# Kernel tuning notes

Measured on AMD Instinct MI355X. Metric: run time of the kernel, lower is better.

Reference implementation:

```python
import jax, jax.numpy as jnp
import numpy as np

V_NUM = 100000
E_NUM = 50000
N_PAIRS = 600000
DIM = 128
TAU = 0.5

def setup_inputs() -> dict:
    key = jax.random.key(0)
    ks = jax.random.split(key, 8)
    v_fea = jax.random.normal(ks[0], (V_NUM, DIM), dtype=jnp.float32)
    t_fea = jax.random.normal(ks[1], (V_NUM, DIM), dtype=jnp.float32)
    e_fea = jax.random.normal(ks[2], (E_NUM, DIM), dtype=jnp.float32)
    # xavier-normal-ish init (gain sqrt(2), fan_in=DIM, fan_out=1)
    std = (2.0 ** 0.5) * (2.0 / (DIM + 1)) ** 0.5
    a_v = jax.random.normal(ks[3], (DIM, 1), dtype=jnp.float32) * std
    a_t = jax.random.normal(ks[4], (DIM, 1), dtype=jnp.float32) * std
    a_e = jax.random.normal(ks[5], (DIM, 1), dtype=jnp.float32) * std
    v_idx = jax.random.randint(ks[6], (N_PAIRS,), 0, V_NUM, dtype=jnp.int32)
    e_idx = jax.random.randint(ks[7], (N_PAIRS,), 0, E_NUM, dtype=jnp.int32)
    ve = jnp.stack([v_idx, e_idx], axis=1)  # [N_PAIRS, 2]
    return {"v_fea": v_fea, "t_fea": t_fea, "e_fea": e_fea,
            "a_v": a_v, "a_t": a_t, "a_e": a_e, "ve": ve}

def reference(v_fea, t_fea, e_fea, a_v, a_t, a_e, ve):
    v = ve[:, 0]
    e = ve[:, 1]
    # per-node / per-edge attention scalars  [*, 1]
    s_v = v_fea @ a_v
    s_t = t_fea @ a_t
    s_e = e_fea @ a_e
    # per-pair score: gather by v and e, tanh, temperature
    a = jnp.tanh(s_v[v] + s_t[v] + s_e[e]) / TAU  # [N_PAIRS, 1]
    # segment softmax over pairs grouped by vertex v
    a_max = jax.ops.segment_max(a, v, num_segments=V_NUM)  # [V_NUM, 1]
    ex = jnp.exp(a - jax.lax.stop_gradient(a_max)[v])
    denom = jax.ops.segment_sum(ex, v, num_segments=V_NUM)  # [V_NUM, 1]
    w = ex / denom[v]  # [N_PAIRS, 1]
    # weighted scatter-sum of edge features into vertices
    out = jax.ops.segment_sum(w * e_fea[e], v, num_segments=V_NUM)  # [V_NUM, DIM]
    return out
```

## Files before the change

kernel.cpp:

```cpp
#include <hip/hip_runtime.h>

#define V_NUM 100000
#define E_NUM 50000
#define N_PAIRS 600000
#define DIM 128
#define SCAN_BLK 1024
#define N_SCAN_BLOCKS ((V_NUM + SCAN_BLK - 1) / SCAN_BLK)

__global__ void scores_kernel(const float* __restrict__ v_fea,
                              const float* __restrict__ t_fea,
                              const float* __restrict__ e_fea,
                              const float* __restrict__ a_v,
                              const float* __restrict__ a_t,
                              const float* __restrict__ a_e,
                              float* __restrict__ s_vt,
                              float* __restrict__ s_e) {
    const int wave = (int)((blockIdx.x * blockDim.x + threadIdx.x) >> 6);
    const int lane = (int)(threadIdx.x & 63);
    if (wave >= V_NUM + E_NUM) return;

    float partial;
    if (wave < V_NUM) {
        const float2 vv = ((const float2*)(v_fea + (size_t)wave * DIM))[lane];
        const float2 tt = ((const float2*)(t_fea + (size_t)wave * DIM))[lane];
        const float2 wv = ((const float2*)a_v)[lane];
        const float2 wt = ((const float2*)a_t)[lane];
        partial = vv.x * wv.x + vv.y * wv.y + tt.x * wt.x + tt.y * wt.y;
    } else {
        const int r = wave - V_NUM;
        const float2 ee = ((const float2*)(e_fea + (size_t)r * DIM))[lane];
        const float2 we = ((const float2*)a_e)[lane];
        partial = ee.x * we.x + ee.y * we.y;
    }
    #pragma unroll
    for (int off = 32; off > 0; off >>= 1)
        partial += __shfl_xor(partial, off, 64);
    if (lane == 0) {
        if (wave < V_NUM) s_vt[wave] = partial;
        else s_e[wave - V_NUM] = partial;
    }
}

__global__ void pair_hist(const int* __restrict__ ve, int* __restrict__ counts) {
    const int p = (int)(blockIdx.x * blockDim.x + threadIdx.x);
    if (p >= N_PAIRS) return;
    const int v = ((const int2*)ve)[p].x;
    atomicAdd(&counts[v], 1);
}

__global__ void scan_blocks(const int* __restrict__ counts,
                            int* __restrict__ blk_scan,
                            int* __restrict__ aux) {
    __shared__ int sdata[256];
    const int tid = (int)threadIdx.x;
    const int base = (int)blockIdx.x * SCAN_BLK + tid * 4;
    int4 c = make_int4(0, 0, 0, 0);
    if (base + 3 < V_NUM) {
        c = *(const int4*)(counts + base);
    } else {
        if (base + 0 < V_NUM) c.x = counts[base + 0];
        if (base + 1 < V_NUM) c.y = counts[base + 1];
        if (base + 2 < V_NUM) c.z = counts[base + 2];
        if (base + 3 < V_NUM) c.w = counts[base + 3];
    }
    const int s = c.x + c.y + c.z + c.w;
    sdata[tid] = s;
    __syncthreads();
    #pragma unroll
    for (int off = 1; off < 256; off <<= 1) {
        const int val = (tid >= off) ? sdata[tid - off] : 0;
        __syncthreads();
        sdata[tid] += val;
        __syncthreads();
    }
    const int excl = sdata[tid] - s;
    if (tid == 255) aux[blockIdx.x] = sdata[255];
    const int e0 = excl;
    const int e1 = e0 + c.x;
    const int e2 = e1 + c.y;
    const int e3 = e2 + c.z;
    if (base + 3 < V_NUM) {
        *(int4*)(blk_scan + base) = make_int4(e0, e1, e2, e3);
    } else {
        if (base + 0 < V_NUM) blk_scan[base + 0] = e0;
        if (base + 1 < V_NUM) blk_scan[base + 1] = e1;
        if (base + 2 < V_NUM) blk_scan[base + 2] = e2;
    }
}

__global__ void scan_aux(int* __restrict__ aux ) {
    __shared__ int sdata[128];
    const int tid = (int)threadIdx.x;
    const int orig = (tid < N_SCAN_BLOCKS) ? aux[tid] : 0;
    sdata[tid] = orig;
    __syncthreads();
    #pragma unroll
    for (int off = 1; off < 128; off <<= 1) {
        const int val = (tid >= off) ? sdata[tid - off] : 0;
        __syncthreads();
        sdata[tid] += val;
        __syncthreads();
    }
    if (tid < N_SCAN_BLOCKS) aux[tid] = sdata[tid] - orig;
}

__global__ void pair_scatter(const int* __restrict__ ve,
                             const float* __restrict__ s_vt,
                             const float* __restrict__ s_e,
                             const int* __restrict__ blk_scan,
                             const int* __restrict__ aux_scan,
                             int* __restrict__ cursor,
                             int* __restrict__ csr_e,
                             float* __restrict__ csr_ex) {
    const int p = (int)(blockIdx.x * blockDim.x + threadIdx.x);
    if (p >= N_PAIRS) return;
    const int2 pe = ((const int2*)ve)[p];
    const int v = pe.x, e = pe.y;
    const float a = tanhf(s_vt[v] + s_e[e]) * 2.0f;
    const float ex = __expf(a);
    const int start = blk_scan[v] + aux_scan[v >> 10];
    const int pos = start + atomicAdd(&cursor[v], 1);
    csr_e[pos] = e;
    csr_ex[pos] = ex;
}

__global__ void csr_aggregate(const int* __restrict__ counts,
                              const int* __restrict__ blk_scan,
                              const int* __restrict__ aux_scan,
                              const int* __restrict__ csr_e,
                              const float* __restrict__ csr_ex,
                              const float* __restrict__ e_fea,
                              float* __restrict__ out) {
    const int v = (int)((blockIdx.x * blockDim.x + threadIdx.x) >> 6);
    const int lane = (int)(threadIdx.x & 63);
    if (v >= V_NUM) return;
    const int start = blk_scan[v] + aux_scan[v >> 10];
    const int cnt = counts[v];

    float denom = 0.0f;
    for (int i = 0; i < cnt; ++i) denom += csr_ex[start + i];
    const float inv = (cnt > 0) ? (1.0f / denom) : 0.0f;

    float2 acc = make_float2(0.0f, 0.0f);
    for (int i = 0; i < cnt; ++i) {
        const int e = csr_e[start + i];
        const float w = csr_ex[start + i] * inv;
        const float2 ef = ((const float2*)(e_fea + (size_t)e * DIM))[lane];
        acc.x += w * ef.x;
        acc.y += w * ef.y;
    }
    ((float2*)(out + (size_t)v * DIM))[lane] = acc;
}

extern "C" void kernel_launch(void* const* d_in, const int* in_sizes, int n_in,
                              void* d_out, int out_size, void* d_ws, size_t ws_size,
                              hipStream_t stream) {
    const float* v_fea = (const float*)d_in[0];
    const float* t_fea = (const float*)d_in[1];
    const float* e_fea = (const float*)d_in[2];
    const float* a_v   = (const float*)d_in[3];
    const float* a_t   = (const float*)d_in[4];
    const float* a_e   = (const float*)d_in[5];
    const int*   ve    = (const int*)d_in[6];
    float* out = (float*)d_out;

    char* ws = (char*)d_ws;
    float* s_vt     = (float*)(ws + 0);
    float* s_e      = (float*)(ws + 524288);
    int*   counts   = (int*)  (ws + 1048576);
    int*   cursor   = (int*)  (ws + 1048576 + 400000);
    int*   blk_scan = (int*)  (ws + 2097152);
    int*   aux_scan = (int*)  (ws + 2097152 + 400000);
    int*   csr_e    = (int*)  (ws + 3145728);
    float* csr_ex   = (float*)(ws + 6291456);

    hipMemsetAsync(counts, 0, 800000, stream);

    {
        const int total_waves = V_NUM + E_NUM;
        const int threads = 256;
        const int blocks = (total_waves * 64 + threads - 1) / threads;
        scores_kernel<<<blocks, threads, 0, stream>>>(v_fea, t_fea, e_fea,
                                                      a_v, a_t, a_e, s_vt, s_e);
    }
    pair_hist<<<(N_PAIRS + 255) / 256, 256, 0, stream>>>(ve, counts);
    scan_blocks<<<N_SCAN_BLOCKS, 256, 0, stream>>>(counts, blk_scan, aux_scan);
    scan_aux<<<1, 128, 0, stream>>>(aux_scan);
    pair_scatter<<<(N_PAIRS + 255) / 256, 256, 0, stream>>>(
        ve, s_vt, s_e, blk_scan, aux_scan, cursor, csr_e, csr_ex);
    {
        const int threads = 256;
        const long long total = (long long)V_NUM * 64;
        const int blocks = (int)((total + threads - 1) / threads);
        csr_aggregate<<<blocks, threads, 0, stream>>>(
            counts, blk_scan, aux_scan, csr_e, csr_ex, e_fea, out);
    }
}
```

Before: 331.9 us.

## Fuse pipeline into one cooperative persistent kernel with grid syncs

Replaces the memset and six separate launches with a single cooperative kernel. It zeroes counts, computes scores, builds the histogram, scans, scatters into the CSR and aggregates, with grid.sync between phases, and keeps the multi-kernel path as a fallback. The CSR entries are packed as int2 (edge, ex) pairs. The aggregation now loads 64 entries per wave at once and broadcasts them with shuffles, which replaces the serial per-lane scalar loads and the separate denominator pass. The aim is to remove launch overhead and the duplicate CSR reads. The cost is a grid-stride persistent schedule and cooperative-launch grid barriers.

After: 1.026 ms. 3.09x slower.

```diff
diff --git a/kernel.cpp b/kernel.cpp
--- a/kernel.cpp
+++ b/kernel.cpp
@@ -1,4 +1,7 @@
 #include <hip/hip_runtime.h>
+#include <hip/hip_cooperative_groups.h>
+
+namespace cg = cooperative_groups;
 
 #define V_NUM 100000
 #define E_NUM 50000
@@ -6,19 +9,152 @@
 #define DIM 128
 #define SCAN_BLK 1024
 #define N_SCAN_BLOCKS ((V_NUM + SCAN_BLK - 1) / SCAN_BLK)
-
-__global__ void scores_kernel(const float* __restrict__ v_fea,
-                              const float* __restrict__ t_fea,
-                              const float* __restrict__ e_fea,
-                              const float* __restrict__ a_v,
-                              const float* __restrict__ a_t,
-                              const float* __restrict__ a_e,
-                              float* __restrict__ s_vt,
-                              float* __restrict__ s_e) {
+#define NTHREADS 256
+
+__global__ __launch_bounds__(NTHREADS, 4)
+void fused_kernel(const float* __restrict__ v_fea, const float* __restrict__ t_fea,
+                  const float* __restrict__ e_fea, const float* __restrict__ a_v,
+                  const float* __restrict__ a_t, const float* __restrict__ a_e,
+                  const int* __restrict__ ve, float* __restrict__ out,
+                  float* __restrict__ s_vt, float* __restrict__ s_e,
+                  int* __restrict__ counts, int* __restrict__ cursor,
+                  int* __restrict__ blk_scan, int* __restrict__ aux_scan,
+                  int2* __restrict__ csr) {
+    cg::grid_group grid = cg::this_grid();
+    __shared__ int sdata[NTHREADS];
+
+    const int tid = (int)(blockIdx.x * blockDim.x + threadIdx.x);
+    const int nthreads = (int)(gridDim.x * blockDim.x);
+    const int lane = (int)(threadIdx.x & 63);
+    const int wid = tid >> 6;
+    const int nwaves = nthreads >> 6;
+
+    {
+        int4* z = (int4*)counts;
+        for (int i = tid; i < 50000; i += nthreads) z[i] = make_int4(0, 0, 0, 0);
+    }
+    {
+        const float2 wv = ((const float2*)a_v)[lane];
+        const float2 wt = ((const float2*)a_t)[lane];
+        const float2 we = ((const float2*)a_e)[lane];
+        for (int row = wid; row < V_NUM + E_NUM; row += nwaves) {
+            float partial;
+            if (row < V_NUM) {
+                const float2 vv = ((const float2*)(v_fea + (size_t)row * DIM))[lane];
+                const float2 tt = ((const float2*)(t_fea + (size_t)row * DIM))[lane];
+                partial = vv.x * wv.x + vv.y * wv.y + tt.x * wt.x + tt.y * wt.y;
+            } else {
+                const int r = row - V_NUM;
+                const float2 ee = ((const float2*)(e_fea + (size_t)r * DIM))[lane];
+                partial = ee.x * we.x + ee.y * we.y;
+            }
+            #pragma unroll
+            for (int off = 32; off; off >>= 1) partial += __shfl_xor(partial, off, 64);
+            if (lane == 0) {
+                if (row < V_NUM) s_vt[row] = partial;
+                else s_e[row - V_NUM] = partial;
+            }
+        }
+    }
+    grid.sync();
+
+    for (int p = tid; p < N_PAIRS; p += nthreads)
+        atomicAdd(&counts[((const int2*)ve)[p].x], 1);
+    grid.sync();
+
+    if (blockIdx.x < N_SCAN_BLOCKS) {
+        const int t = (int)threadIdx.x;
+        const int base = (int)blockIdx.x * SCAN_BLK + t * 4;
+        int4 c = make_int4(0, 0, 0, 0);
+        if (base + 3 < V_NUM) {
+            c = *(const int4*)(counts + base);
+        } else {
+            if (base + 0 < V_NUM) c.x = counts[base + 0];
+            if (base + 1 < V_NUM) c.y = counts[base + 1];
+            if (base + 2 < V_NUM) c.z = counts[base + 2];
+            if (base + 3 < V_NUM) c.w = counts[base + 3];
+        }
+        const int s = c.x + c.y + c.z + c.w;
+        sdata[t] = s;
+        __syncthreads();
+        #pragma unroll
+        for (int off = 1; off < NTHREADS; off <<= 1) {
+            const int val = (t >= off) ? sdata[t - off] : 0;
+            __syncthreads();
+            sdata[t] += val;
+            __syncthreads();
+        }
+        const int excl = sdata[t] - s;
+        if (t == NTHREADS - 1) aux_scan[blockIdx.x] = sdata[NTHREADS - 1];
+        const int e0 = excl, e1 = e0 + c.x, e2 = e1 + c.y, e3 = e2 + c.z;
+        if (base + 3 < V_NUM) {
+            *(int4*)(blk_scan + base) = make_int4(e0, e1, e2, e3);
+        } else {
+            if (base + 0 < V_NUM) blk_scan[base + 0] = e0;
+            if (base + 1 < V_NUM) blk_scan[base + 1] = e1;
+            if (base + 2 < V_NUM) blk_scan[base + 2] = e2;
+        }
+    }
+    grid.sync();
+
+    if (blockIdx.x == 0) {
+        const int t = (int)threadIdx.x;
+        const int orig = (t < N_SCAN_BLOCKS) ? aux_scan[t] : 0;
+        sdata[t] = orig;
+        __syncthreads();
+        #pragma unroll
+        for (int off = 1; off < NTHREADS; off <<= 1) {
+            const int val = (t >= off) ? sdata[t - off] : 0;
+            __syncthreads();
+            sdata[t] += val;
+            __syncthreads();
+        }
+        if (t < N_SCAN_BLOCKS) aux_scan[t] = sdata[t] - orig;
+    }
+    grid.sync();
+
+    for (int p = tid; p < N_PAIRS; p += nthreads) {
+        const int2 pe = ((const int2*)ve)[p];
+        const float a = tanhf(s_vt[pe.x] + s_e[pe.y]) * 2.0f;
+        const float ex = __expf(a);
+        const int pos = blk_scan[pe.x] + aux_scan[pe.x >> 10] + atomicAdd(&cursor[pe.x], 1);
+        csr[pos] = make_int2(pe.y, __float_as_int(ex));
+    }
+    grid.sync();
+
+    for (int v = wid; v < V_NUM; v += nwaves) {
+        const int start = blk_scan[v] + aux_scan[v >> 10];
+        const int cnt = counts[v];
+        float2 acc = make_float2(0.0f, 0.0f);
+        float denom = 0.0f;
+        for (int base = 0; base < cnt; base += 64) {
+            const int m = min(64, cnt - base);
+            int2 ent = make_int2(0, 0);
+            if (lane < m) ent = csr[start + base + lane];
+            float exv = (lane < m) ? __int_as_float(ent.y) : 0.0f;
+            #pragma unroll
+            for (int off = 32; off; off >>= 1) exv += __shfl_xor(exv, off, 64);
+            denom += exv;
+            for (int i = 0; i < m; ++i) {
+                const int e = __shfl(ent.x, i, 64);
+                const float w = __int_as_float(__shfl(ent.y, i, 64));
+                const float2 ef = ((const float2*)(e_fea + (size_t)e * DIM))[lane];
+                acc.x += w * ef.x;
+                acc.y += w * ef.y;
+            }
+        }
+        const float inv = (cnt > 0) ? (1.0f / denom) : 0.0f;
+        ((float2*)(out + (size_t)v * DIM))[lane] = make_float2(acc.x * inv, acc.y * inv);
+    }
+}
+
+__global__ void scores_kernel(const float* __restrict__ v_fea, const float* __restrict__ t_fea,
+                              const float* __restrict__ e_fea, const float* __restrict__ a_v,
+                              const float* __restrict__ a_t, const float* __restrict__ a_e,
+                              float* __restrict__ s_vt, float* __restrict__ s_e) {
     const int wave = (int)((blockIdx.x * blockDim.x + threadIdx.x) >> 6);
     const int lane = (int)(threadIdx.x & 63);
     if (wave >= V_NUM + E_NUM) return;
-
     float partial;
     if (wave < V_NUM) {
         const float2 vv = ((const float2*)(v_fea + (size_t)wave * DIM))[lane];
@@ -33,8 +169,7 @@
         partial = ee.x * we.x + ee.y * we.y;
     }
     #pragma unroll
-    for (int off = 32; off > 0; off >>= 1)
-        partial += __shfl_xor(partial, off, 64);
+    for (int off = 32; off; off >>= 1) partial += __shfl_xor(partial, off, 64);
     if (lane == 0) {
         if (wave < V_NUM) s_vt[wave] = partial;
         else s_e[wave - V_NUM] = partial;
@@ -44,20 +179,17 @@
 __global__ void pair_hist(const int* __restrict__ ve, int* __restrict__ counts) {
     const int p = (int)(blockIdx.x * blockDim.x + threadIdx.x);
     if (p >= N_PAIRS) return;
-    const int v = ((const int2*)ve)[p].x;
-    atomicAdd(&counts[v], 1);
-}
-
-__global__ void scan_blocks(const int* __restrict__ counts,
-                            int* __restrict__ blk_scan,
+    atomicAdd(&counts[((const int2*)ve)[p].x], 1);
+}
+
+__global__ void scan_blocks(const int* __restrict__ counts, int* __restrict__ blk_scan,
                             int* __restrict__ aux) {
     __shared__ int sdata[256];
     const int tid = (int)threadIdx.x;
     const int base = (int)blockIdx.x * SCAN_BLK + tid * 4;
     int4 c = make_int4(0, 0, 0, 0);
-    if (base + 3 < V_NUM) {
-        c = *(const int4*)(counts + base);
-    } else {
+    if (base + 3 < V_NUM) c = *(const int4*)(counts + base);
+    else {
         if (base + 0 < V_NUM) c.x = counts[base + 0];
         if (base + 1 < V_NUM) c.y = counts[base + 1];
         if (base + 2 < V_NUM) c.z = counts[base + 2];
@@ -75,20 +207,16 @@
     }
     const int excl = sdata[tid] - s;
     if (tid == 255) aux[blockIdx.x] = sdata[255];
-    const int e0 = excl;
-    const int e1 = e0 + c.x;
-    const int e2 = e1 + c.y;
-    const int e3 = e2 + c.z;
-    if (base + 3 < V_NUM) {
-        *(int4*)(blk_scan + base) = make_int4(e0, e1, e2, e3);
-    } else {
+    const int e0 = excl, e1 = e0 + c.x, e2 = e1 + c.y, e3 = e2 + c.z;
+    if (base + 3 < V_NUM) *(int4*)(blk_scan + base) = make_int4(e0, e1, e2, e3);
+    else {
         if (base + 0 < V_NUM) blk_scan[base + 0] = e0;
         if (base + 1 < V_NUM) blk_scan[base + 1] = e1;
         if (base + 2 < V_NUM) blk_scan[base + 2] = e2;
     }
 }
 
-__global__ void scan_aux(int* __restrict__ aux ) {
+__global__ void scan_aux(int* __restrict__ aux) {
     __shared__ int sdata[128];
     const int tid = (int)threadIdx.x;
     const int orig = (tid < N_SCAN_BLOCKS) ? aux[tid] : 0;
@@ -104,52 +232,47 @@
     if (tid < N_SCAN_BLOCKS) aux[tid] = sdata[tid] - orig;
 }
 
-__global__ void pair_scatter(const int* __restrict__ ve,
-                             const float* __restrict__ s_vt,
-                             const float* __restrict__ s_e,
-                             const int* __restrict__ blk_scan,
-                             const int* __restrict__ aux_scan,
-                             int* __restrict__ cursor,
-                             int* __restrict__ csr_e,
-                             float* __restrict__ csr_ex) {
+__global__ void pair_scatter(const int* __restrict__ ve, const float* __restrict__ s_vt,
+                             const float* __restrict__ s_e, const int* __restrict__ blk_scan,
+                             const int* __restrict__ aux_scan, int* __restrict__ cursor,
+                             int2* __restrict__ csr) {
     const int p = (int)(blockIdx.x * blockDim.x + threadIdx.x);
     if (p >= N_PAIRS) return;
     const int2 pe = ((const int2*)ve)[p];
-    const int v = pe.x, e = pe.y;
-    const float a = tanhf(s_vt[v] + s_e[e]) * 2.0f;
+    const float a = tanhf(s_vt[pe.x] + s_e[pe.y]) * 2.0f;
     const float ex = __expf(a);
-    const int start = blk_scan[v] + aux_scan[v >> 10];
-    const int pos = start + atomicAdd(&cursor[v], 1);
-    csr_e[pos] = e;
-    csr_ex[pos] = ex;
-}
-
-__global__ void csr_aggregate(const int* __restrict__ counts,
-                              const int* __restrict__ blk_scan,
-                              const int* __restrict__ aux_scan,
-                              const int* __restrict__ csr_e,
-                              const float* __restrict__ csr_ex,
-                              const float* __restrict__ e_fea,
-                              float* __restrict__ out) {
+    const int pos = blk_scan[pe.x] + aux_scan[pe.x >> 10] + atomicAdd(&cursor[pe.x], 1);
+    csr[pos] = make_int2(pe.y, __float_as_int(ex));
+}
+
+__global__ void csr_aggregate(const int* __restrict__ counts, const int* __restrict__ blk_scan,
+                              const int* __restrict__ aux_scan, const int2* __restrict__ csr,
+                              const float* __restrict__ e_fea, float* __restrict__ out) {
     const int v = (int)((blockIdx.x * blockDim.x + threadIdx.x) >> 6);
     const int lane = (int)(threadIdx.x & 63);
     if (v >= V_NUM) return;
     const int start = blk_scan[v] + aux_scan[v >> 10];
     const int cnt = counts[v];
-
+    float2 acc = make_float2(0.0f, 0.0f);
     float denom = 0.0f;
-    for (int i = 0; i < cnt; ++i) denom += csr_ex[start + i];
+    for (int base = 0; base < cnt; base += 64) {
+        const int m = min(64, cnt - base);
+        int2 ent = make_int2(0, 0);
+        if (lane < m) ent = csr[start + base + lane];
+        float exv = (lane < m) ? __int_as_float(ent.y) : 0.0f;
+        #pragma unroll
+        for (int off = 32; off; off >>= 1) exv += __shfl_xor(exv, off, 64);
+        denom += exv;
+        for (int i = 0; i < m; ++i) {
+            const int e = __shfl(ent.x, i, 64);
+            const float w = __int_as_float(__shfl(ent.y, i, 64));
+            const float2 ef = ((const float2*)(e_fea + (size_t)e * DIM))[lane];
+            acc.x += w * ef.x;
+            acc.y += w * ef.y;
+        }
+    }
     const float inv = (cnt > 0) ? (1.0f / denom) : 0.0f;
-
-    float2 acc = make_float2(0.0f, 0.0f);
-    for (int i = 0; i < cnt; ++i) {
-        const int e = csr_e[start + i];
-        const float w = csr_ex[start + i] * inv;
-        const float2 ef = ((const float2*)(e_fea + (size_t)e * DIM))[lane];
-        acc.x += w * ef.x;
-        acc.y += w * ef.y;
-    }
-    ((float2*)(out + (size_t)v * DIM))[lane] = acc;
+    ((float2*)(out + (size_t)v * DIM))[lane] = make_float2(acc.x * inv, acc.y * inv);
 }
 
 extern "C" void kernel_launch(void* const* d_in, const int* in_sizes, int n_in,
@@ -171,28 +294,41 @@
     int*   cursor   = (int*)  (ws + 1048576 + 400000);
     int*   blk_scan = (int*)  (ws + 2097152);
     int*   aux_scan = (int*)  (ws + 2097152 + 400000);
-    int*   csr_e    = (int*)  (ws + 3145728);
-    float* csr_ex   = (float*)(ws + 6291456);
-
-    hipMemsetAsync(counts, 0, 800000, stream);
-
-    {
-        const int total_waves = V_NUM + E_NUM;
-        const int threads = 256;
-        const int blocks = (total_waves * 64 + threads - 1) / threads;
-        scores_kernel<<<blocks, threads, 0, stream>>>(v_fea, t_fea, e_fea,
-                                                      a_v, a_t, a_e, s_vt, s_e);
-    }
-    pair_hist<<<(N_PAIRS + 255) / 256, 256, 0, stream>>>(ve, counts);
-    scan_blocks<<<N_SCAN_BLOCKS, 256, 0, stream>>>(counts, blk_scan, aux_scan);
-    scan_aux<<<1, 128, 0, stream>>>(aux_scan);
-    pair_scatter<<<(N_PAIRS + 255) / 256, 256, 0, stream>>>(
-        ve, s_vt, s_e, blk_scan, aux_scan, cursor, csr_e, csr_ex);
-    {
-        const int threads = 256;
-        const long long total = (long long)V_NUM * 64;
-        const int blocks = (int)((total + threads - 1) / threads);
-        csr_aggregate<<<blocks, threads, 0, stream>>>(
-            counts, blk_scan, aux_scan, csr_e, csr_ex, e_fea, out);
-    }
-}
+    int2*  csr      = (int2*) (ws + 3145728);
+
+    int maxBlocksPerCU = 0;
+    hipError_t qerr = hipOccupancyMaxActiveBlocksPerMultiprocessor(
+        &maxBlocksPerCU, fused_kernel, NTHREADS, 0);
+    int grid = (qerr == hipSuccess && maxBlocksPerCU > 0) ? maxBlocksPerCU * 256 : 0;
+    if (grid > 2048) grid = 2048;
+
+    bool launched = false;
+    if (grid >= N_SCAN_BLOCKS) {
+        void* args[] = {(void*)&v_fea, (void*)&t_fea, (void*)&e_fea, (void*)&a_v,
+                        (void*)&a_t, (void*)&a_e, (void*)&ve, (void*)&out,
+                        (void*)&s_vt, (void*)&s_e, (void*)&counts, (void*)&cursor,
+                        (void*)&blk_scan, (void*)&aux_scan, (void*)&csr};
+        hipError_t err = hipLaunchCooperativeKernel(fused_kernel, dim3(grid), dim3(NTHREADS),
+                                                    args, 0, stream);
+        launched = (err == hipSuccess);
+    }
+
+    if (!launched) {
+        hipMemsetAsync(counts, 0, 800000, stream);
+        {
+            const int total_waves = V_NUM + E_NUM;
+            scores_kernel<<<(total_waves * 64 + 255) / 256, 256, 0, stream>>>(
+                v_fea, t_fea, e_fea, a_v, a_t, a_e, s_vt, s_e);
+        }
+        pair_hist<<<(N_PAIRS + 255) / 256, 256, 0, stream>>>(ve, counts);
+        scan_blocks<<<N_SCAN_BLOCKS, 256, 0, stream>>>(counts, blk_scan, aux_scan);
+        scan_aux<<<1, 128, 0, stream>>>(aux_scan);
+        pair_scatter<<<(N_PAIRS + 255) / 256, 256, 0, stream>>>(
+            ve, s_vt, s_e, blk_scan, aux_scan, cursor, csr);
+        {
+            const long long total = (long long)V_NUM * 64;
+            csr_aggregate<<<(int)((total + 255) / 256), 256, 0, stream>>>(
+                counts, blk_scan, aux_scan, csr, e_fea, out);
+        }
+    }
+}
```
